# Performance work log

Measured on AMD Instinct MI355X. Metric: run time of the kernel, lower is better.

## Reference

```python
import jax, jax.numpy as jnp
import numpy as np

N, H, V, MAX_STEPS = 256, 128, 64, 4

def setup_inputs() -> dict:
    key = jax.random.key(0)
    ks = jax.random.split(key, 16)
    def w(k, shape, fan_in):
        return jax.random.normal(k, shape, dtype=jnp.float32) / np.sqrt(fan_in)
    inp = {}
    inp['node_embeddings'] = jax.random.normal(ks[0], (N, H), dtype=jnp.float32)
    inp['skip_embeddings'] = jax.random.normal(ks[1], (N, N, H), dtype=jnp.float32)
    inp['Wx'] = w(ks[2], (H, 4 * H), H)
    inp['Wh'] = w(ks[3], (H, 4 * H), H)
    inp['b'] = jnp.zeros((4 * H,), jnp.float32)
    inp['Wxs'] = w(ks[4], (H, 4 * H), H)
    inp['Whs'] = w(ks[5], (H, 4 * H), H)
    inp['bs'] = jnp.zeros((4 * H,), jnp.float32)
    inp['Wb'] = w(ks[6], (2 * H, 2), 2 * H)
    inp['bb'] = jnp.zeros((2,), jnp.float32)
    inp['Wk'] = w(ks[7], (H, H), H)
    inp['bk'] = jnp.zeros((H,), jnp.float32)
    inp['Wq'] = w(ks[8], (2 * H, H), 2 * H)
    inp['bq'] = jnp.zeros((H,), jnp.float32)
    inp['Wl'] = w(ks[9], (2 * H, 1), 2 * H)
    inp['bl'] = jnp.zeros((1,), jnp.float32)
    inp['Wd'] = w(ks[10], (2 * H, V), 2 * H)
    inp['bd'] = jnp.zeros((V,), jnp.float32)
    # valid skips only forward in the program (include diagonal = no-skip)
    inp['skip_mask'] = jnp.triu(jnp.ones((N, N), dtype=bool))
    inp['true_indexes'] = jax.random.randint(ks[11], (N,), 0, N, dtype=jnp.int32)
    inp['false_indexes'] = jax.random.randint(ks[12], (N,), 0, N, dtype=jnp.int32)
    inp['exit_index'] = N - 1
    return inp

def _lstm(c, h, x, Wx, Wh, b):
    gates = x @ Wx + h @ Wh + b  # [..., 4H]
    i, f, g, o = jnp.split(gates, 4, axis=-1)
    c2 = jax.nn.sigmoid(f) * c + jax.nn.sigmoid(i) * jnp.tanh(g)
    h2 = jax.nn.sigmoid(o) * jnp.tanh(c2)
    return c2, h2

def reference(node_embeddings, skip_embeddings, Wx, Wh, b, Wxs, Whs, bs,
              Wb, bb, Wk, bk, Wq, bq, Wl, bl, Wd, bd,
              skip_mask, true_indexes, false_indexes, exit_index):
    n, hdim = node_embeddings.shape
    eye = jnp.eye(n, dtype=node_embeddings.dtype)
    ip0 = jnp.zeros((n,), node_embeddings.dtype).at[0].set(1.0)
    c0 = jnp.zeros((n, hdim), node_embeddings.dtype)
    h0 = jnp.zeros((n, hdim), node_embeddings.dtype)
    keys = skip_embeddings @ Wk + bk  # [N,N,H] (input-only, precompute)

    def step(carry, _):
        ip, c, h = carry
        # per-node LSTM proposals
        c_p, h_p = _lstm(c, h, node_embeddings, Wx, Wh, b)  # [N,H]
        hid = jnp.concatenate([c_p, h_p], axis=-1)  # [N,2H]
        # skip proposals: carry of source i applied to skip embedding (i,j)
        c_sk, h_sk = _lstm(c[:, None, :], h[:, None, :], skip_embeddings, Wxs, Whs, bs)  # [N,N,H]
        # branch decisions
        branch = jax.nn.softmax(hid @ Wb + bb, axis=-1)  # [N,2]
        # skip decisions (per source i, softmax over destinations j)
        queries = hid @ Wq + bq  # [N,H]
        kq = jax.nn.relu(jnp.concatenate(
            [keys, jnp.broadcast_to(queries[:, None, :], (n, n, hdim))], axis=-1))  # [N,N,2H]
        logits = jnp.einsum('ijk,kl->ijl', kq, Wl)[..., 0] + bl[0]  # [N,N]
        skip_dec = jax.nn.softmax(jnp.where(skip_mask, logits, -jnp.inf), axis=-1)
        # aggregation (IPA)
        yes_skip = skip_dec * (1.0 - eye)  # zero diagonal
        no_skip = jnp.diagonal(skip_dec)
        p_bt = ip * no_skip * branch[:, 0]
        p_bf = ip * no_skip * branch[:, 1]
        new_ip = (jax.ops.segment_sum(p_bt, true_indexes, num_segments=n)
                  + jax.ops.segment_sum(p_bf, false_indexes, num_segments=n)
                  + jnp.einsum('i,ij->j', ip, yes_skip))
        denom = new_ip[:, None] + 1e-7
        def agg(hp, hsk):
            t = jax.ops.segment_sum(hp * p_bt[:, None], true_indexes, num_segments=n)
            f = jax.ops.segment_sum(hp * p_bf[:, None], false_indexes, num_segments=n)
            s = jnp.einsum('ijh,i,ij->jh', hsk, ip, yes_skip)
            return (t + f + s) / denom
        return (new_ip, agg(c_p, c_sk), agg(h_p, h_sk)), None

    (ip, c, h), _ = jax.lax.scan(step, (ip0, c0, h0), None, length=MAX_STEPS)
    exit_concat = jnp.concatenate([c[exit_index], h[exit_index]], axis=-1)  # [2H]
    return exit_concat @ Wd + bd  # [V]
```

## Files before the change

### kernel.cpp

```cpp
#include <hip/hip_runtime.h>
#include <hip/hip_bf16.h>

constexpr int NN = 256;
constexpr int HH = 128;
constexpr int GG = 512;
constexpr int NP = NN * NN;

typedef __attribute__((ext_vector_type(8))) short short8;
typedef __attribute__((ext_vector_type(4))) float f32x4;

__device__ unsigned short g_xs[(size_t)NP * GG];
__device__ unsigned short g_wfr[20 * 512 * 8];
__device__ float g_bsp[GG];
__device__ float g_pwh[HH * HH * 4];
__device__ float g_pws[HH * HH * 4];
__device__ float g_kterm[NP];
__device__ float g_yesw[NP];
__device__ float g_noskip[NN];
__device__ float g_xg[NN * HH * 4];
__device__ float g_xga[NN * HH * 4];
__device__ float g_hws[NN * HH * 4];
__device__ float g_c[NN * HH];
__device__ float g_h[NN * HH];
__device__ float g_sc[NN * HH];
__device__ float g_sh[NN * HH];
__device__ float g_ip[NN];
__device__ float g_nip[NN];

__device__ __forceinline__ unsigned short f2bf(float f) {
  unsigned int u = __float_as_uint(f);
  u = (u + 0x7fffu + ((u >> 16) & 1u)) >> 16;
  return (unsigned short)u;
}
__device__ __forceinline__ float bf2f(unsigned short s) {
  return __uint_as_float(((unsigned int)s) << 16);
}
__device__ __forceinline__ float frcp(float x) {
#if __has_builtin(__builtin_amdgcn_rcpf)
  return __builtin_amdgcn_rcpf(x);
#else
  return 1.0f / x;
#endif
}
__device__ __forceinline__ float sigm(float x) { return frcp(1.f + __expf(-x)); }
__device__ __forceinline__ float tanhfast(float x) { return 1.f - 2.f * frcp(__expf(2.f * x) + 1.f); }

__global__ void k_init() {
  int idx = blockIdx.x * blockDim.x + threadIdx.x;
  g_sc[idx] = 0.f; g_sh[idx] = 0.f; g_c[idx] = 0.f; g_h[idx] = 0.f;
  *(float4*)&g_hws[(size_t)idx * 4] = make_float4(0.f, 0.f, 0.f, 0.f);
  if (idx < NN) { g_nip[idx] = 0.f; g_ip[idx] = (idx == 0) ? 1.f : 0.f; }
}

__global__ __launch_bounds__(512) void k_prep(const float* __restrict__ Wxs,
                                              const float* __restrict__ Wk,
                                              const float* __restrict__ bs) {
  const int bidx = blockIdx.x;
  const int tile = bidx >> 2, ks = bidx & 3;
  const int s = threadIdx.x;
  const int ct = s >> 6, l = s & 63;
  const int c = ct * 16 + (l & 15);
  const int kbase = ks * 32 + (l >> 4) * 8;
  int src = 0;
  if (tile < 4) src = (c & 3) * 128 + tile * 32 + (c >> 2);
  unsigned short* dst = &g_wfr[((size_t)bidx * 512 + s) * 8];
#pragma unroll
  for (int e = 0; e < 8; ++e) {
    int k = kbase + e;
    float v = (tile < 4) ? Wxs[k * GG + src] : Wk[k * HH + c];
    dst[e] = f2bf(v);
  }
  if (tile < 4 && ks == 0 && (l >> 4) == 0) g_bsp[tile * 128 + c] = bs[src];
}

__global__ __launch_bounds__(128) void k_prep2(const float* __restrict__ Wh,
                                               const float* __restrict__ Whs) {
  const int k = blockIdx.x, t = threadIdx.x;
  float4 a = make_float4(Wh[k * GG + t], Wh[k * GG + 128 + t], Wh[k * GG + 256 + t], Wh[k * GG + 384 + t]);
  float4 s = make_float4(Whs[k * GG + t], Whs[k * GG + 128 + t], Whs[k * GG + 256 + t], Whs[k * GG + 384 + t]);
  *(float4*)&g_pwh[((size_t)k * HH + t) * 4] = a;
  *(float4*)&g_pws[((size_t)k * HH + t) * 4] = s;
}

__global__ __launch_bounds__(128) void k_xg(const float* __restrict__ NE,
                                            const float* __restrict__ Wx,
                                            const float* __restrict__ b) {
  const int i = blockIdx.x, t = threadIdx.x;
  __shared__ float ne[HH];
  ne[t] = NE[i * HH + t];
  __syncthreads();
  float a0 = b[t], a1 = b[128 + t], a2 = b[256 + t], a3 = b[384 + t];
  for (int k = 0; k < HH; ++k) {
    float x = ne[k];
    a0 = fmaf(x, Wx[k * GG + t], a0);
    a1 = fmaf(x, Wx[k * GG + 128 + t], a1);
    a2 = fmaf(x, Wx[k * GG + 256 + t], a2);
    a3 = fmaf(x, Wx[k * GG + 384 + t], a3);
  }
  float4 v = make_float4(a0, a1, a2, a3);
  *(float4*)&g_xg[((size_t)i * HH + t) * 4] = v;
  *(float4*)&g_xga[((size_t)i * HH + t) * 4] = v;
}

__device__ __forceinline__ void loadB(short8* dst, int tile, int ks, int l) {
  const unsigned short* wf = &g_wfr[((size_t)(tile * 4 + ks)) * 4096 + l * 8];
#pragma unroll
  for (int ct = 0; ct < 8; ++ct) dst[ct] = *(const short8*)(wf + ct * 512);
}

__global__ __launch_bounds__(256) void k_gemm(const float* __restrict__ SE,
                                              const float* __restrict__ bk,
                                              const float* __restrict__ Wl) {
  __shared__ __align__(16) char lds[32768];
  const int bid = blockIdx.x;
  const int tile = blockIdx.y;
  const int pb = (bid < 128) ? (bid * 2) : ((bid - 128) * 2 + 1);
  const int pairBase = pb * 128;
  const int tid = threadIdx.x;

  for (int cc = tid; cc < 2048; cc += 256) {
    int row = cc >> 4, kc = cc & 15;
    const float* src = SE + (size_t)(pairBase + row) * HH + kc * 8;
    float4 f0 = *(const float4*)(src);
    float4 f1 = *(const float4*)(src + 4);
    short8 v;
    v[0] = (short)f2bf(f0.x); v[1] = (short)f2bf(f0.y); v[2] = (short)f2bf(f0.z); v[3] = (short)f2bf(f0.w);
    v[4] = (short)f2bf(f1.x); v[5] = (short)f2bf(f1.y); v[6] = (short)f2bf(f1.z); v[7] = (short)f2bf(f1.w);
    *(short8*)(lds + row * 256 + ((kc * 16) ^ ((row & 7) << 4))) = v;
  }
  __syncthreads();

  const int wv = tid >> 6;
  const int l = tid & 63;
  const int l15 = l & 15, lg = l >> 4;

  f32x4 acc[2][8];
#pragma unroll
  for (int rt = 0; rt < 2; ++rt)
#pragma unroll
    for (int ct = 0; ct < 8; ++ct) acc[rt][ct] = (f32x4){0.f, 0.f, 0.f, 0.f};

  short8 bA[8], bB[8];
  loadB(bA, tile, 0, l);
#pragma unroll
  for (int ks = 0; ks < 4; ks += 2) {
    loadB(bB, tile, ks + 1, l);
    {
      const int kb = ks * 64 + lg * 16;
      short8 a[2];
#pragma unroll
      for (int rt = 0; rt < 2; ++rt) {
        int row = wv * 32 + rt * 16 + l15;
        a[rt] = *(const short8*)(lds + row * 256 + (kb ^ ((row & 7) << 4)));
      }
#pragma unroll
      for (int rt = 0; rt < 2; ++rt)
#pragma unroll
        for (int ct = 0; ct < 8; ++ct)
          acc[rt][ct] = __builtin_amdgcn_mfma_f32_16x16x32_bf16(a[rt], bA[ct], acc[rt][ct], 0, 0, 0);
    }
    if (ks + 2 < 4) loadB(bA, tile, ks + 2, l);
    {
      const int kb = (ks + 1) * 64 + lg * 16;
      short8 a[2];
#pragma unroll
      for (int rt = 0; rt < 2; ++rt) {
        int row = wv * 32 + rt * 16 + l15;
        a[rt] = *(const short8*)(lds + row * 256 + (kb ^ ((row & 7) << 4)));
      }
#pragma unroll
      for (int rt = 0; rt < 2; ++rt)
#pragma unroll
        for (int ct = 0; ct < 8; ++ct)
          acc[rt][ct] = __builtin_amdgcn_mfma_f32_16x16x32_bf16(a[rt], bB[ct], acc[rt][ct], 0, 0, 0);
    }
  }

  if (tile < 4) {
#pragma unroll
    for (int rt = 0; rt < 2; ++rt)
#pragma unroll
      for (int ct = 0; ct < 8; ++ct) {
        const int col = ct * 16 + l15;
        const float bsv = g_bsp[tile * 128 + col];
#pragma unroll
        for (int r = 0; r < 4; ++r) {
          int row = wv * 32 + rt * 16 + lg * 4 + r;
          int pair = pairBase + row;
          int jj = pair & 255, ii = pair >> 8;
          if (jj > ii) g_xs[(size_t)pair * GG + tile * 128 + col] = f2bf(acc[rt][ct][r] + bsv);
        }
      }
  } else {
#pragma unroll
    for (int rt = 0; rt < 2; ++rt) {
#pragma unroll
      for (int r = 0; r < 4; ++r) {
        float s = 0.f;
#pragma unroll
        for (int ct = 0; ct < 8; ++ct) {
          int col = ct * 16 + l15;
          float x = acc[rt][ct][r] + bk[col];
          x = fmaxf(x, 0.f);
          s = fmaf(x, Wl[col], s);
        }
#pragma unroll
        for (int m = 1; m < 16; m <<= 1) s += __shfl_xor(s, m, 64);
        int row = wv * 32 + rt * 16 + lg * 4 + r;
        int pair = pairBase + row;
        int jj = pair & 255, ii = pair >> 8;
        if (l15 == 0 && jj >= ii) g_kterm[pair] = s;
      }
    }
  }
}

__global__ __launch_bounds__(256) void k_softmax() {
  const int i = blockIdx.x, j = threadIdx.x;
  __shared__ float sm[NN];
  float x = -1e30f;
  if (j >= i) x = g_kterm[i * NN + j];
  sm[j] = x;
  __syncthreads();
  for (int s = 128; s > 0; s >>= 1) { if (j < s) sm[j] = fmaxf(sm[j], sm[j + s]); __syncthreads(); }
  float mx = sm[0];
  __syncthreads();
  float e = (j >= i) ? __expf(x - mx) : 0.f;
  sm[j] = e;
  __syncthreads();
  for (int s = 128; s > 0; s >>= 1) { if (j < s) sm[j] += sm[j + s]; __syncthreads(); }
  float p = e * frcp(sm[0]);
  g_yesw[i * NN + j] = (j == i) ? 0.f : p;
  if (j == i) g_noskip[i] = p;
}

__global__ __launch_bounds__(128) void k_step(const float* __restrict__ Wb,
                                              const float* __restrict__ bb,
                                              const int* __restrict__ tix,
                                              const int* __restrict__ fix) {
  const int t = threadIdx.x;
  if (blockIdx.x < 256) {
    const int i = blockIdx.x;
    __shared__ float red[2][2];
    const float4 a = *(const float4*)&g_xga[((size_t)i * HH + t) * 4];
    float co = g_c[i * HH + t];
    float c2 = sigm(a.y) * co + sigm(a.x) * tanhfast(a.z);
    float h2 = sigm(a.w) * tanhfast(c2);
    float q0 = c2 * Wb[2 * t] + h2 * Wb[2 * (128 + t)];
    float q1 = c2 * Wb[2 * t + 1] + h2 * Wb[2 * (128 + t) + 1];
#pragma unroll
    for (int m = 1; m < 64; m <<= 1) { q0 += __shfl_xor(q0, m, 64); q1 += __shfl_xor(q1, m, 64); }
    if ((t & 63) == 0) { red[t >> 6][0] = q0; red[t >> 6][1] = q1; }
    __syncthreads();
    float l0 = red[0][0] + red[1][0] + bb[0];
    float l1 = red[0][1] + red[1][1] + bb[1];
    float mm = fmaxf(l0, l1);
    float e0 = __expf(l0 - mm), e1 = __expf(l1 - mm);
    float inv = frcp(e0 + e1);
    float ipv = g_ip[i] * g_noskip[i];
    if (ipv != 0.f) {
      float pbt = ipv * e0 * inv, pbf = ipv * e1 * inv;
      int ti = tix[i], fi = fix[i];
      atomicAdd(&g_sc[ti * HH + t], c2 * pbt);
      atomicAdd(&g_sh[ti * HH + t], h2 * pbt);
      atomicAdd(&g_sc[fi * HH + t], c2 * pbf);
      atomicAdd(&g_sh[fi * HH + t], h2 * pbf);
      if (t == 0) { atomicAdd(&g_nip[ti], pbt); atomicAdd(&g_nip[fi], pbf); }
    }
  } else {
    const int idx = blockIdx.x - 256;
    const int j = idx >> 4, chunk = idx & 15;
    const int i0 = chunk * 16;
    if (i0 >= j) return;
    const int iN = (j - i0 < 16) ? (j - i0) : 16;
    __shared__ float wsh[16];
    if (t < 16) wsh[t] = (t < iN) ? g_ip[i0 + t] * g_yesw[(i0 + t) * NN + j] : 0.f;
    __syncthreads();
    float accC = 0.f, accH = 0.f, accW = 0.f;
    for (int ii = 0; ii < iN; ++ii) {
      float wgt = wsh[ii];
      if (wgt == 0.f) continue;
      const int i = i0 + ii;
      const ushort4 gv = *(const ushort4*)&g_xs[((size_t)(i * NN + j) * 128 + t) * 4];
      float4 hw = *(const float4*)&g_hws[((size_t)i * HH + t) * 4];
      float xi = bf2f(gv.x) + hw.x;
      float xf = bf2f(gv.y) + hw.y;
      float xg = bf2f(gv.z) + hw.z;
      float xo = bf2f(gv.w) + hw.w;
      float c2 = sigm(xf) * g_c[i * HH + t] + sigm(xi) * tanhfast(xg);
      float h2 = sigm(xo) * tanhfast(c2);
      accC = fmaf(wgt, c2, accC);
      accH = fmaf(wgt, h2, accH);
      accW += wgt;
    }
    if (accW != 0.f) {
      atomicAdd(&g_sc[j * HH + t], accC);
      atomicAdd(&g_sh[j * HH + t], accH);
      if (t == 0) atomicAdd(&g_nip[j], accW);
    }
  }
}

__global__ __launch_bounds__(512) void k_finish(const int last) {
  const int j = blockIdx.x, tid = threadIdx.x;
  const int t = tid & 127, sel = tid >> 7;
  __shared__ float hsm[HH];
  __shared__ float4 part[4][HH];
  if (sel == 0) {
    float nip = g_nip[j];
    float d = frcp(nip + 1e-7f);
    float cv = g_sc[j * HH + t] * d;
    float hv = g_sh[j * HH + t] * d;
    g_c[j * HH + t] = cv;
    g_h[j * HH + t] = hv;
    hsm[t] = hv;
    g_sc[j * HH + t] = 0.f;
    g_sh[j * HH + t] = 0.f;
    if (t == 0) { g_ip[j] = nip; g_nip[j] = 0.f; }
  }
  __syncthreads();
  if (last) return;
  const float* __restrict__ W = (sel >> 1) ? g_pws : g_pwh;
  const int k0 = (sel & 1) * 64;
  float s0 = 0.f, s1 = 0.f, s2 = 0.f, s3 = 0.f;
#pragma unroll 8
  for (int k = k0; k < k0 + 64; ++k) {
    float hk = hsm[k];
    const float4 w = *(const float4*)&W[((size_t)k * HH + t) * 4];
    s0 = fmaf(hk, w.x, s0); s1 = fmaf(hk, w.y, s1);
    s2 = fmaf(hk, w.z, s2); s3 = fmaf(hk, w.w, s3);
  }
  part[sel][t] = make_float4(s0, s1, s2, s3);
  __syncthreads();
  if (sel == 0) {
    float4 p0 = part[0][t], p1 = part[1][t];
    float4 xg = *(const float4*)&g_xg[((size_t)j * HH + t) * 4];
    *(float4*)&g_xga[((size_t)j * HH + t) * 4] =
        make_float4(xg.x + p0.x + p1.x, xg.y + p0.y + p1.y,
                    xg.z + p0.z + p1.z, xg.w + p0.w + p1.w);
  } else if (sel == 2) {
    float4 p2 = part[2][t], p3 = part[3][t];
    *(float4*)&g_hws[((size_t)j * HH + t) * 4] =
        make_float4(p2.x + p3.x, p2.y + p3.y, p2.z + p3.z, p2.w + p3.w);
  }
}

__global__ __launch_bounds__(64) void k_out(const float* __restrict__ Wd,
                                            const float* __restrict__ bd,
                                            const int* __restrict__ ei,
                                            float* __restrict__ out) {
  const int v = threadIdx.x;
  const int e = ei[0];
  float s = bd[v];
  for (int h = 0; h < HH; ++h) {
    s = fmaf(g_c[e * HH + h], Wd[h * 64 + v], s);
    s = fmaf(g_h[e * HH + h], Wd[(128 + h) * 64 + v], s);
  }
  out[v] = s;
}

extern "C" void kernel_launch(void* const* d_in, const int* in_sizes, int n_in,
                              void* d_out, int out_size, void* d_ws, size_t ws_size,
                              hipStream_t stream) {
  const float* NE  = (const float*)d_in[0];
  const float* SE  = (const float*)d_in[1];
  const float* Wx  = (const float*)d_in[2];
  const float* Wh  = (const float*)d_in[3];
  const float* b   = (const float*)d_in[4];
  const float* Wxs = (const float*)d_in[5];
  const float* Whs = (const float*)d_in[6];
  const float* bs  = (const float*)d_in[7];
  const float* Wb  = (const float*)d_in[8];
  const float* bb  = (const float*)d_in[9];
  const float* Wk  = (const float*)d_in[10];
  const float* bk  = (const float*)d_in[11];
  const float* Wl  = (const float*)d_in[14];
  const float* Wd  = (const float*)d_in[16];
  const float* bd  = (const float*)d_in[17];
  const int* tix = (const int*)d_in[19];
  const int* fix = (const int*)d_in[20];
  const int* ei  = (const int*)d_in[21];
  float* out = (float*)d_out;

  k_init<<<256, 128, 0, stream>>>();
  k_prep<<<20, 512, 0, stream>>>(Wxs, Wk, bs);
  k_prep2<<<128, 128, 0, stream>>>(Wh, Whs);
  k_xg<<<256, 128, 0, stream>>>(NE, Wx, b);
  k_gemm<<<dim3(384, 5), 256, 0, stream>>>(SE, bk, Wl);
  k_softmax<<<256, 256, 0, stream>>>();
  for (int s = 0; s < 4; ++s) {
    k_step<<<256 + 4096, 128, 0, stream>>>(Wb, bb, tix, fix);
    k_finish<<<256, 512, 0, stream>>>(s == 3);
  }
  k_out<<<1, 64, 0, stream>>>(Wd, bd, ei, out);
}
```

Measured before the change: 156.4 us.

## Fuse prep kernels, transpose skip layouts, replace skip atomics with chunk partials

Merges the four setup kernels into one launch. Transposes the stored skip gate inputs and skip weights so each destination j reads its sources contiguously. Cuts the skip work into 8 chunks of 32 sources instead of 16 chunks of 16, with each chunk writing a private partial instead of issuing atomicAdds. k_finish then sums those partials and handles 4 destination rows per block, so each recurrent weight load is shared across 4 rows. This trades atomic contention and launch overhead for extra partial-buffer traffic and less parallelism in the finish and skip kernels.

```diff
diff --git a/kernel.cpp b/kernel.cpp
--- a/kernel.cpp
+++ b/kernel.cpp
@@ -5,6 +5,8 @@
 constexpr int HH = 128;
 constexpr int GG = 512;
 constexpr int NP = NN * NN;
+constexpr int NCH = 8;
+constexpr int CHSZ = 32;
 
 typedef __attribute__((ext_vector_type(8))) short short8;
 typedef __attribute__((ext_vector_type(4))) float f32x4;
@@ -15,7 +17,7 @@
 __device__ float g_pwh[HH * HH * 4];
 __device__ float g_pws[HH * HH * 4];
 __device__ float g_kterm[NP];
-__device__ float g_yesw[NP];
+__device__ float g_yeswT[NP];
 __device__ float g_noskip[NN];
 __device__ float g_xg[NN * HH * 4];
 __device__ float g_xga[NN * HH * 4];
@@ -24,6 +26,9 @@
 __device__ float g_h[NN * HH];
 __device__ float g_sc[NN * HH];
 __device__ float g_sh[NN * HH];
+__device__ float g_pc[NCH * NN * HH];
+__device__ float g_ph[NCH * NN * HH];
+__device__ float g_pw[NCH * NN];
 __device__ float g_ip[NN];
 __device__ float g_nip[NN];
 
@@ -45,61 +50,61 @@
 __device__ __forceinline__ float sigm(float x) { return frcp(1.f + __expf(-x)); }
 __device__ __forceinline__ float tanhfast(float x) { return 1.f - 2.f * frcp(__expf(2.f * x) + 1.f); }
 
-__global__ void k_init() {
-  int idx = blockIdx.x * blockDim.x + threadIdx.x;
-  g_sc[idx] = 0.f; g_sh[idx] = 0.f; g_c[idx] = 0.f; g_h[idx] = 0.f;
-  *(float4*)&g_hws[(size_t)idx * 4] = make_float4(0.f, 0.f, 0.f, 0.f);
-  if (idx < NN) { g_nip[idx] = 0.f; g_ip[idx] = (idx == 0) ? 1.f : 0.f; }
-}
-
-__global__ __launch_bounds__(512) void k_prep(const float* __restrict__ Wxs,
-                                              const float* __restrict__ Wk,
-                                              const float* __restrict__ bs) {
-  const int bidx = blockIdx.x;
-  const int tile = bidx >> 2, ks = bidx & 3;
-  const int s = threadIdx.x;
-  const int ct = s >> 6, l = s & 63;
-  const int c = ct * 16 + (l & 15);
-  const int kbase = ks * 32 + (l >> 4) * 8;
-  int src = 0;
-  if (tile < 4) src = (c & 3) * 128 + tile * 32 + (c >> 2);
-  unsigned short* dst = &g_wfr[((size_t)bidx * 512 + s) * 8];
-#pragma unroll
-  for (int e = 0; e < 8; ++e) {
-    int k = kbase + e;
-    float v = (tile < 4) ? Wxs[k * GG + src] : Wk[k * HH + c];
-    dst[e] = f2bf(v);
-  }
-  if (tile < 4 && ks == 0 && (l >> 4) == 0) g_bsp[tile * 128 + c] = bs[src];
-}
-
-__global__ __launch_bounds__(128) void k_prep2(const float* __restrict__ Wh,
-                                               const float* __restrict__ Whs) {
-  const int k = blockIdx.x, t = threadIdx.x;
-  float4 a = make_float4(Wh[k * GG + t], Wh[k * GG + 128 + t], Wh[k * GG + 256 + t], Wh[k * GG + 384 + t]);
-  float4 s = make_float4(Whs[k * GG + t], Whs[k * GG + 128 + t], Whs[k * GG + 256 + t], Whs[k * GG + 384 + t]);
-  *(float4*)&g_pwh[((size_t)k * HH + t) * 4] = a;
-  *(float4*)&g_pws[((size_t)k * HH + t) * 4] = s;
-}
-
-__global__ __launch_bounds__(128) void k_xg(const float* __restrict__ NE,
-                                            const float* __restrict__ Wx,
-                                            const float* __restrict__ b) {
-  const int i = blockIdx.x, t = threadIdx.x;
-  __shared__ float ne[HH];
-  ne[t] = NE[i * HH + t];
-  __syncthreads();
-  float a0 = b[t], a1 = b[128 + t], a2 = b[256 + t], a3 = b[384 + t];
-  for (int k = 0; k < HH; ++k) {
-    float x = ne[k];
-    a0 = fmaf(x, Wx[k * GG + t], a0);
-    a1 = fmaf(x, Wx[k * GG + 128 + t], a1);
-    a2 = fmaf(x, Wx[k * GG + 256 + t], a2);
-    a3 = fmaf(x, Wx[k * GG + 384 + t], a3);
-  }
-  float4 v = make_float4(a0, a1, a2, a3);
-  *(float4*)&g_xg[((size_t)i * HH + t) * 4] = v;
-  *(float4*)&g_xga[((size_t)i * HH + t) * 4] = v;
+__global__ __launch_bounds__(512) void k_pre(const float* __restrict__ NE,
+                                             const float* __restrict__ Wx,
+                                             const float* __restrict__ b,
+                                             const float* __restrict__ Wxs,
+                                             const float* __restrict__ Wk,
+                                             const float* __restrict__ bs,
+                                             const float* __restrict__ Wh,
+                                             const float* __restrict__ Whs) {
+  const int bid = blockIdx.x;
+  const int tid = threadIdx.x;
+  if (bid < 64) {
+    const int idx = bid * 512 + tid;
+    g_sc[idx] = 0.f; g_sh[idx] = 0.f; g_c[idx] = 0.f; g_h[idx] = 0.f;
+    *(float4*)&g_hws[(size_t)idx * 4] = make_float4(0.f, 0.f, 0.f, 0.f);
+    if (idx < NN) { g_nip[idx] = 0.f; g_ip[idx] = (idx == 0) ? 1.f : 0.f; }
+  } else if (bid < 84) {
+    const int bidx = bid - 64;
+    const int tile = bidx >> 2, ks = bidx & 3;
+    const int ct = tid >> 6, l = tid & 63;
+    const int c = ct * 16 + (l & 15);
+    const int kbase = ks * 32 + (l >> 4) * 8;
+    int src = 0;
+    if (tile < 4) src = (c & 3) * 128 + tile * 32 + (c >> 2);
+    unsigned short* dst = &g_wfr[((size_t)bidx * 512 + tid) * 8];
+#pragma unroll
+    for (int e = 0; e < 8; ++e) {
+      int k = kbase + e;
+      float v = (tile < 4) ? Wxs[k * GG + src] : Wk[k * HH + c];
+      dst[e] = f2bf(v);
+    }
+    if (tile < 4 && ks == 0 && (l >> 4) == 0) g_bsp[tile * 128 + c] = bs[src];
+  } else if (bid < 116) {
+    const int k = (bid - 84) * 4 + (tid >> 7), t = tid & 127;
+    float4 a = make_float4(Wh[k * GG + t], Wh[k * GG + 128 + t], Wh[k * GG + 256 + t], Wh[k * GG + 384 + t]);
+    float4 s = make_float4(Whs[k * GG + t], Whs[k * GG + 128 + t], Whs[k * GG + 256 + t], Whs[k * GG + 384 + t]);
+    *(float4*)&g_pwh[((size_t)k * HH + t) * 4] = a;
+    *(float4*)&g_pws[((size_t)k * HH + t) * 4] = s;
+  } else {
+    __shared__ float ne[4][HH];
+    const int sub = tid >> 7, t = tid & 127;
+    const int i = (bid - 116) * 4 + sub;
+    ne[sub][t] = NE[i * HH + t];
+    __syncthreads();
+    float a0 = b[t], a1 = b[128 + t], a2 = b[256 + t], a3 = b[384 + t];
+    for (int k = 0; k < HH; ++k) {
+      float x = ne[sub][k];
+      a0 = fmaf(x, Wx[k * GG + t], a0);
+      a1 = fmaf(x, Wx[k * GG + 128 + t], a1);
+      a2 = fmaf(x, Wx[k * GG + 256 + t], a2);
+      a3 = fmaf(x, Wx[k * GG + 384 + t], a3);
+    }
+    float4 v = make_float4(a0, a1, a2, a3);
+    *(float4*)&g_xg[((size_t)i * HH + t) * 4] = v;
+    *(float4*)&g_xga[((size_t)i * HH + t) * 4] = v;
+  }
 }
 
 __device__ __forceinline__ void loadB(short8* dst, int tile, int ks, int l) {
@@ -188,7 +193,8 @@
           int row = wv * 32 + rt * 16 + lg * 4 + r;
           int pair = pairBase + row;
           int jj = pair & 255, ii = pair >> 8;
-          if (jj > ii) g_xs[(size_t)pair * GG + tile * 128 + col] = f2bf(acc[rt][ct][r] + bsv);
+          if (jj > ii)
+            g_xs[((size_t)jj * NN + ii) * GG + tile * 128 + col] = f2bf(acc[rt][ct][r] + bsv);
         }
       }
   } else {
@@ -230,7 +236,7 @@
   __syncthreads();
   for (int s = 128; s > 0; s >>= 1) { if (j < s) sm[j] += sm[j + s]; __syncthreads(); }
   float p = e * frcp(sm[0]);
-  g_yesw[i * NN + j] = (j == i) ? 0.f : p;
+  g_yeswT[j * NN + i] = (j == i) ? 0.f : p;
   if (j == i) g_noskip[i] = p;
 }
 
@@ -269,19 +275,19 @@
     }
   } else {
     const int idx = blockIdx.x - 256;
-    const int j = idx >> 4, chunk = idx & 15;
-    const int i0 = chunk * 16;
+    const int j = idx >> 3, ch = idx & 7;
+    const int i0 = ch * CHSZ;
     if (i0 >= j) return;
-    const int iN = (j - i0 < 16) ? (j - i0) : 16;
-    __shared__ float wsh[16];
-    if (t < 16) wsh[t] = (t < iN) ? g_ip[i0 + t] * g_yesw[(i0 + t) * NN + j] : 0.f;
+    const int iN = (j - i0 < CHSZ) ? (j - i0) : CHSZ;
+    __shared__ float wsh[CHSZ];
+    if (t < CHSZ) wsh[t] = (t < iN) ? g_ip[i0 + t] * g_yeswT[j * NN + i0 + t] : 0.f;
     __syncthreads();
     float accC = 0.f, accH = 0.f, accW = 0.f;
     for (int ii = 0; ii < iN; ++ii) {
       float wgt = wsh[ii];
       if (wgt == 0.f) continue;
       const int i = i0 + ii;
-      const ushort4 gv = *(const ushort4*)&g_xs[((size_t)(i * NN + j) * 128 + t) * 4];
+      const ushort4 gv = *(const ushort4*)&g_xs[((size_t)j * NN + i) * GG + t * 4];
       float4 hw = *(const float4*)&g_hws[((size_t)i * HH + t) * 4];
       float xi = bf2f(gv.x) + hw.x;
       float xf = bf2f(gv.y) + hw.y;
@@ -293,55 +299,74 @@
       accH = fmaf(wgt, h2, accH);
       accW += wgt;
     }
-    if (accW != 0.f) {
-      atomicAdd(&g_sc[j * HH + t], accC);
-      atomicAdd(&g_sh[j * HH + t], accH);
-      if (t == 0) atomicAdd(&g_nip[j], accW);
-    }
-  }
-}
-
-__global__ __launch_bounds__(512) void k_finish(const int last) {
-  const int j = blockIdx.x, tid = threadIdx.x;
-  const int t = tid & 127, sel = tid >> 7;
-  __shared__ float hsm[HH];
-  __shared__ float4 part[4][HH];
-  if (sel == 0) {
+    g_pc[((size_t)ch * NN + j) * HH + t] = accC;
+    g_ph[((size_t)ch * NN + j) * HH + t] = accH;
+    if (t == 0) g_pw[ch * NN + j] = accW;
+  }
+}
+
+__global__ __launch_bounds__(256) void k_finish(const int last) {
+  const int j0 = blockIdx.x * 4;
+  const int tid = threadIdx.x;
+  __shared__ float hsm[4][HH];
+  __shared__ float nipsh[4];
+  if (tid < 4) {
+    const int j = j0 + tid;
     float nip = g_nip[j];
-    float d = frcp(nip + 1e-7f);
-    float cv = g_sc[j * HH + t] * d;
-    float hv = g_sh[j * HH + t] * d;
+    const int nch = (j + 31) >> 5;
+    for (int ch = 0; ch < nch; ++ch) nip += g_pw[ch * NN + j];
+    nipsh[tid] = nip;
+    g_ip[j] = nip;
+    g_nip[j] = 0.f;
+  }
+  __syncthreads();
+#pragma unroll
+  for (int s = 0; s < 2; ++s) {
+    const int slot = tid + s * 256;
+    const int jj = slot >> 7, t = slot & 127;
+    const int j = j0 + jj;
+    float sc = g_sc[j * HH + t], sh = g_sh[j * HH + t];
+    const int nch = (j + 31) >> 5;
+    for (int ch = 0; ch < nch; ++ch) {
+      sc += g_pc[((size_t)ch * NN + j) * HH + t];
+      sh += g_ph[((size_t)ch * NN + j) * HH + t];
+    }
+    float d = frcp(nipsh[jj] + 1e-7f);
+    float cv = sc * d, hv = sh * d;
     g_c[j * HH + t] = cv;
     g_h[j * HH + t] = hv;
-    hsm[t] = hv;
+    hsm[jj][t] = hv;
     g_sc[j * HH + t] = 0.f;
     g_sh[j * HH + t] = 0.f;
-    if (t == 0) { g_ip[j] = nip; g_nip[j] = 0.f; }
   }
   __syncthreads();
   if (last) return;
-  const float* __restrict__ W = (sel >> 1) ? g_pws : g_pwh;
-  const int k0 = (sel & 1) * 64;
-  float s0 = 0.f, s1 = 0.f, s2 = 0.f, s3 = 0.f;
-#pragma unroll 8
-  for (int k = k0; k < k0 + 64; ++k) {
-    float hk = hsm[k];
+  const int m = tid >> 7, t = tid & 127;
+  const float* __restrict__ W = m ? g_pws : g_pwh;
+  float4 a0 = make_float4(0.f, 0.f, 0.f, 0.f), a1 = a0, a2 = a0, a3 = a0;
+#pragma unroll 4
+  for (int k = 0; k < HH; ++k) {
     const float4 w = *(const float4*)&W[((size_t)k * HH + t) * 4];
-    s0 = fmaf(hk, w.x, s0); s1 = fmaf(hk, w.y, s1);
-    s2 = fmaf(hk, w.z, s2); s3 = fmaf(hk, w.w, s3);
-  }
-  part[sel][t] = make_float4(s0, s1, s2, s3);
-  __syncthreads();
-  if (sel == 0) {
-    float4 p0 = part[0][t], p1 = part[1][t];
-    float4 xg = *(const float4*)&g_xg[((size_t)j * HH + t) * 4];
-    *(float4*)&g_xga[((size_t)j * HH + t) * 4] =
-        make_float4(xg.x + p0.x + p1.x, xg.y + p0.y + p1.y,
-                    xg.z + p0.z + p1.z, xg.w + p0.w + p1.w);
-  } else if (sel == 2) {
-    float4 p2 = part[2][t], p3 = part[3][t];
-    *(float4*)&g_hws[((size_t)j * HH + t) * 4] =
-        make_float4(p2.x + p3.x, p2.y + p3.y, p2.z + p3.z, p2.w + p3.w);
+    const float h0 = hsm[0][k], h1 = hsm[1][k], h2 = hsm[2][k], h3 = hsm[3][k];
+    a0.x = fmaf(h0, w.x, a0.x); a0.y = fmaf(h0, w.y, a0.y); a0.z = fmaf(h0, w.z, a0.z); a0.w = fmaf(h0, w.w, a0.w);
+    a1.x = fmaf(h1, w.x, a1.x); a1.y = fmaf(h1, w.y, a1.y); a1.z = fmaf(h1, w.z, a1.z); a1.w = fmaf(h1, w.w, a1.w);
+    a2.x = fmaf(h2, w.x, a2.x); a2.y = fmaf(h2, w.y, a2.y); a2.z = fmaf(h2, w.z, a2.z); a2.w = fmaf(h2, w.w, a2.w);
+    a3.x = fmaf(h3, w.x, a3.x); a3.y = fmaf(h3, w.y, a3.y); a3.z = fmaf(h3, w.z, a3.z); a3.w = fmaf(h3, w.w, a3.w);
+  }
+  if (m == 0) {
+    float4 x0 = *(const float4*)&g_xg[((size_t)(j0 + 0) * HH + t) * 4];
+    float4 x1 = *(const float4*)&g_xg[((size_t)(j0 + 1) * HH + t) * 4];
+    float4 x2 = *(const float4*)&g_xg[((size_t)(j0 + 2) * HH + t) * 4];
+    float4 x3 = *(const float4*)&g_xg[((size_t)(j0 + 3) * HH + t) * 4];
+    *(float4*)&g_xga[((size_t)(j0 + 0) * HH + t) * 4] = make_float4(x0.x + a0.x, x0.y + a0.y, x0.z + a0.z, x0.w + a0.w);
+    *(float4*)&g_xga[((size_t)(j0 + 1) * HH + t) * 4] = make_float4(x1.x + a1.x, x1.y + a1.y, x1.z + a1.z, x1.w + a1.w);
+    *(float4*)&g_xga[((size_t)(j0 + 2) * HH + t) * 4] = make_float4(x2.x + a2.x, x2.y + a2.y, x2.z + a2.z, x2.w + a2.w);
+    *(float4*)&g_xga[((size_t)(j0 + 3) * HH + t) * 4] = make_float4(x3.x + a3.x, x3.y + a3.y, x3.z + a3.z, x3.w + a3.w);
+  } else {
+    *(float4*)&g_hws[((size_t)(j0 + 0) * HH + t) * 4] = a0;
+    *(float4*)&g_hws[((size_t)(j0 + 1) * HH + t) * 4] = a1;
+    *(float4*)&g_hws[((size_t)(j0 + 2) * HH + t) * 4] = a2;
+    *(float4*)&g_hws[((size_t)(j0 + 3) * HH + t) * 4] = a3;
   }
 }
 
@@ -382,15 +407,12 @@
   const int* ei  = (const int*)d_in[21];
   float* out = (float*)d_out;
 
-  k_init<<<256, 128, 0, stream>>>();
-  k_prep<<<20, 512, 0, stream>>>(Wxs, Wk, bs);
-  k_prep2<<<128, 128, 0, stream>>>(Wh, Whs);
-  k_xg<<<256, 128, 0, stream>>>(NE, Wx, b);
+  k_pre<<<180, 512, 0, stream>>>(NE, Wx, b, Wxs, Wk, bs, Wh, Whs);
   k_gemm<<<dim3(384, 5), 256, 0, stream>>>(SE, bk, Wl);
   k_softmax<<<256, 256, 0, stream>>>();
   for (int s = 0; s < 4; ++s) {
-    k_step<<<256 + 4096, 128, 0, stream>>>(Wb, bb, tix, fix);
-    k_finish<<<256, 512, 0, stream>>>(s == 3);
+    k_step<<<256 + NN * NCH, 128, 0, stream>>>(Wb, bb, tix, fix);
+    k_finish<<<64, 256, 0, stream>>>(s == 3);
   }
   k_out<<<1, 64, 0, stream>>>(Wd, bd, ei, out);
 }
```

After: 179.7 us. 1.15x slower.
